# Optimization experiments

Measured on AMD Instinct MI355X. Metric: run time of the kernel, lower is better.

Reference implementation:

```python
import jax, jax.numpy as jnp
import numpy as np

EPS = 1e-8


def setup_inputs() -> dict:
    key = jax.random.key(0)
    k1, k2, k3, k4 = jax.random.split(key, 4)
    B, S, H, D, E = 2, 2048, 1024, 4096, 8
    x = jax.random.normal(k1, (B, S, H), dtype=jnp.float32)
    routing_weights = jax.random.uniform(k2, (B, S, E), dtype=jnp.float32)
    # xavier-uniform-like scale for the expert weight tensors
    lim_d = float(np.sqrt(6.0 / (H + D)))
    lim_u = float(np.sqrt(6.0 / (D + H)))
    down_weights = jax.random.uniform(k3, (E, H, D), dtype=jnp.float32, minval=-lim_d, maxval=lim_d)
    up_weights = jax.random.uniform(k4, (E, D, H), dtype=jnp.float32, minval=-lim_u, maxval=lim_u)
    down_biases = jnp.zeros((E, D), dtype=jnp.float32)
    return {
        "x": x,
        "routing_weights": routing_weights,
        "down_weights": down_weights,
        "down_biases": down_biases,
        "up_weights": up_weights,
        "top_k": 2,
    }


def reference(x, routing_weights, down_weights, down_biases, up_weights, top_k):
    """SmearExpert.forward with routing_strategy='top_k_sparse' (3D routing weights).
    Returns (output, sparse_weights) exactly as the torch module does."""
    B, S, H = x.shape
    E = down_weights.shape[0]

    # top-k sparsification + renormalization of the routing weights
    topk_w, topk_i = jax.lax.top_k(routing_weights, top_k)          # [B,S,k]
    sparse_w = (jax.nn.one_hot(topk_i, E, dtype=x.dtype) * topk_w[..., None]).sum(-2)  # [B,S,E]
    sparse_w = sparse_w / (sparse_w.sum(-1, keepdims=True) + EPS)

    x_flat = x.reshape(-1, H)              # [T,H]
    w_flat = sparse_w.reshape(-1, E)       # [T,E]

    # per-expert down-proj -> GELU(exact) -> up-proj, combined with routing weights
    # (tokens with zero weight contribute nothing, matching the masked torch path)
    out = jnp.zeros_like(x_flat)
    for e in range(E):
        z = jax.nn.gelu(x_flat @ down_weights[e] + down_biases[e], approximate=False)  # [T,D]
        out = out + (z @ up_weights[e]) * w_flat[:, e:e + 1]
    return out.reshape(B, S, H), sparse_w
```

## Files before the change

kernel.cpp:

```cpp
#include <hip/hip_runtime.h>
#include <stdint.h>

#define T_TOK 4096
#define HDIM  1024
#define DDIM  4096
#define NEXP  8

typedef unsigned short ushort_t;
typedef __attribute__((ext_vector_type(8))) short bf16x8;
typedef __attribute__((ext_vector_type(4))) float f32x4;

__device__ __forceinline__ float bf2f(ushort_t b) {
  return __uint_as_float(((unsigned int)b) << 16);
}
__device__ __forceinline__ unsigned int f2bf(float f) {
  unsigned int u = __float_as_uint(f);
  return (u + 0x7fffu + ((u >> 16) & 1u)) >> 16;
}

__device__ __forceinline__ void gld16(const void* g, void* l) {
  __builtin_amdgcn_global_load_lds(
      (const __attribute__((address_space(1))) unsigned int*)g,
      (__attribute__((address_space(3))) unsigned int*)l, 16, 0, 0);
}

__global__ void k_init(int* counts) {
  if (threadIdx.x < NEXP) counts[threadIdx.x] = 0;
}

__global__ void k_route(const float* __restrict__ rw, float* __restrict__ sw_out,
                        int* counts, int* inv_e, int* inv_p, float* inv_w,
                        int* tokA) {
  int t = blockIdx.x * 256 + threadIdx.x;
  if (t >= T_TOK) return;
  float v[NEXP];
#pragma unroll
  for (int e = 0; e < NEXP; e++) v[e] = rw[t * NEXP + e];
  int i0 = 0; float m0 = v[0];
#pragma unroll
  for (int e = 1; e < NEXP; e++) if (v[e] > m0) { m0 = v[e]; i0 = e; }
  int i1 = -1; float m1 = -1e30f;
#pragma unroll
  for (int e = 0; e < NEXP; e++) if (e != i0 && v[e] > m1) { m1 = v[e]; i1 = e; }
  float s = m0 + m1 + 1e-8f;
  float w0 = m0 / s, w1 = m1 / s;
#pragma unroll
  for (int e = 0; e < NEXP; e++) {
    float w = (e == i0) ? w0 : ((e == i1) ? w1 : 0.0f);
    sw_out[t * NEXP + e] = w;
  }
  int p0 = atomicAdd(&counts[i0], 1);
  int p1 = atomicAdd(&counts[i1], 1);
  tokA[i0 * T_TOK + p0] = t;
  tokA[i1 * T_TOK + p1] = t;
  inv_e[t * 2] = i0; inv_e[t * 2 + 1] = i1;
  inv_p[t * 2] = p0; inv_p[t * 2 + 1] = p1;
  inv_w[t * 2] = w0; inv_w[t * 2 + 1] = w1;
}

__global__ void k_offsets(const int* counts, int* offsets) {
  int acc = 0;
  for (int e = 0; e < NEXP; e++) { offsets[e] = acc; acc += counts[e]; }
}

__global__ __launch_bounds__(256)
void k_cvtx(const float* __restrict__ x, ushort_t* __restrict__ xb) {
  size_t i = (size_t)blockIdx.x * 256 + threadIdx.x;
  float4 f0 = ((const float4*)x)[i * 2];
  float4 f1 = ((const float4*)x)[i * 2 + 1];
  uint4 o;
  o.x = f2bf(f0.x) | (f2bf(f0.y) << 16);
  o.y = f2bf(f0.z) | (f2bf(f0.w) << 16);
  o.z = f2bf(f1.x) | (f2bf(f1.y) << 16);
  o.w = f2bf(f1.z) | (f2bf(f1.w) << 16);
  ((uint4*)xb)[i] = o;
}

template <int KDIM, int NDIM>
__global__ __launch_bounds__(256)
void k_cvtw(const float* __restrict__ W, ushort_t* __restrict__ Wt) {
  constexpr int KT = KDIM / 64;
  __shared__ __align__(16) ushort_t lds[64 * 256];
  const int ekt = blockIdx.y;
  const int e  = ekt / KT;
  const int kt = ekt % KT;
  const int n0 = blockIdx.x * 256;
  const int t  = threadIdx.x;
  const int wv = t >> 6;
  const int ln = t & 63;
  const float* src = W + (size_t)e * KDIM * NDIM + (size_t)(kt * 64) * NDIM + n0;
#pragma unroll
  for (int it = 0; it < 16; ++it) {
    int r = it * 4 + wv;
    float4 f = *(const float4*)(src + (size_t)r * NDIM + ln * 4);
    uint2 o;
    o.x = f2bf(f.x) | (f2bf(f.y) << 16);
    o.y = f2bf(f.z) | (f2bf(f.w) << 16);
    *(uint2*)(lds + r * 256 + ln * 4) = o;
  }
  __syncthreads();
  ushort_t* dst = Wt + ((size_t)ekt * NDIM + n0 + t) * 64;
  const int sw = t & 7;
#pragma unroll
  for (int g = 0; g < 8; ++g) {
    unsigned int h0 = lds[(g * 8 + 0) * 256 + t];
    unsigned int h1 = lds[(g * 8 + 1) * 256 + t];
    unsigned int h2 = lds[(g * 8 + 2) * 256 + t];
    unsigned int h3 = lds[(g * 8 + 3) * 256 + t];
    unsigned int h4 = lds[(g * 8 + 4) * 256 + t];
    unsigned int h5 = lds[(g * 8 + 5) * 256 + t];
    unsigned int h6 = lds[(g * 8 + 6) * 256 + t];
    unsigned int h7 = lds[(g * 8 + 7) * 256 + t];
    uint4 o;
    o.x = h0 | (h1 << 16);
    o.y = h2 | (h3 << 16);
    o.z = h4 | (h5 << 16);
    o.w = h6 | (h7 << 16);
    *(uint4*)(dst + (g ^ sw) * 8) = o;
  }
}

template <int KDIM, int NDIM, bool DOWN>
__global__ __launch_bounds__(256, 3)
void k_gemm(const ushort_t* __restrict__ Asrc, const ushort_t* __restrict__ Wt,
            const float* __restrict__ bias, const int* __restrict__ counts,
            const int* __restrict__ offsets, const int* __restrict__ tokA,
            ushort_t* __restrict__ Out) {
  constexpr int KT = KDIM / 64;
  __shared__ __align__(16) short a_sh[128 * 64];
  __shared__ __align__(16) short b_sh[128 * 64];
  const int e    = blockIdx.y >> 5;
  const int tile = blockIdx.y & 31;
  const int cnt  = counts[e];
  if (tile * 128 >= cnt) return;
  const int off_e = offsets[e];
  const int zbase = off_e + tile * 128;
  const int n0    = blockIdx.x * 128;
  const int tid   = threadIdx.x;
  const int wave  = tid >> 6;
  const int lane  = tid & 63;
  const int rgrp  = lane >> 3;
  const int lc    = lane & 7;

  const ushort_t* abase[4];
#pragma unroll
  for (int i = 0; i < 4; i++) {
    int rl = wave * 32 + i * 8 + rgrp;
    int ridx = tile * 128 + rl;
    int ridx_c = (ridx < cnt) ? ridx : tile * 128;
    size_t row;
    if constexpr (DOWN) row = (size_t)tokA[e * T_TOK + ridx_c];
    else                row = (size_t)(off_e + ridx_c);
    abase[i] = Asrc + row * KDIM + ((lc ^ (rl & 7)) * 8);
  }
  const ushort_t* bbase = Wt + ((size_t)e * KT * NDIM + n0) * 64 + wave * 2048 + lane * 8;
  char* a_seg = (char*)a_sh + wave * 4096;
  char* b_seg = (char*)b_sh + wave * 4096;

  const int lm   = lane & 15;
  const int quad = lane >> 4;

  f32x4 acc[8][2];
  const f32x4 zero = {0.0f, 0.0f, 0.0f, 0.0f};
#pragma unroll
  for (int mf = 0; mf < 8; mf++)
#pragma unroll
    for (int nf = 0; nf < 2; nf++) acc[mf][nf] = zero;

  for (int kt = 0; kt < KT; ++kt) {
#pragma unroll
    for (int it = 0; it < 4; ++it)
      gld16(abase[it] + kt * 64, a_seg + it * 1024);
    const ushort_t* bg = bbase + (size_t)kt * (NDIM * 64);
#pragma unroll
    for (int it = 0; it < 4; ++it)
      gld16(bg + it * 512, b_seg + it * 1024);
    __syncthreads();
#pragma unroll
    for (int ks = 0; ks < 2; ++ks) {
      bf16x8 af[8];
#pragma unroll
      for (int mf = 0; mf < 8; mf++) {
        int m = mf * 16 + lm;
        int cc = (ks * 4 + quad) ^ (lm & 7);
        af[mf] = *(const bf16x8*)(a_sh + m * 64 + cc * 8);
      }
      bf16x8 bfv[2];
#pragma unroll
      for (int nf = 0; nf < 2; nf++) {
        int n = wave * 32 + nf * 16 + lm;
        int cc = (ks * 4 + quad) ^ (lm & 7);
        bfv[nf] = *(const bf16x8*)(b_sh + n * 64 + cc * 8);
      }
#pragma unroll
      for (int mf = 0; mf < 8; mf++)
#pragma unroll
        for (int nf = 0; nf < 2; nf++)
          acc[mf][nf] = __builtin_amdgcn_mfma_f32_16x16x32_bf16(af[mf], bfv[nf], acc[mf][nf], 0, 0, 0);
    }
    __syncthreads();
  }

  float bv[2] = {0.0f, 0.0f};
  if constexpr (DOWN) {
#pragma unroll
    for (int nf = 0; nf < 2; nf++)
      bv[nf] = bias[e * NDIM + n0 + wave * 32 + nf * 16 + lm];
  }
  short* ep = ((wave & 2) ? b_sh : a_sh) + (wave & 1) * 4096;
#pragma unroll
  for (int mf = 0; mf < 8; mf++)
#pragma unroll
    for (int nf = 0; nf < 2; nf++)
#pragma unroll
      for (int r = 0; r < 4; r++) {
        float v = acc[mf][nf][r];
        if constexpr (DOWN) {
          float zv = v + bv[nf];
          v = 0.5f * zv * (1.0f + erff(zv * 0.70710678118654752f));
        }
        ep[(mf * 16 + quad * 4 + r) * 32 + nf * 16 + lm] = (short)f2bf(v);
      }
  __syncthreads();
#pragma unroll
  for (int it = 0; it < 8; ++it) {
    int row = it * 16 + (lane >> 2);
    uint4 v = *(const uint4*)(ep + row * 32 + (lane & 3) * 8);
    if (tile * 128 + row < cnt)
      *(uint4*)(Out + (size_t)(zbase + row) * NDIM + n0 + wave * 32 + (lane & 3) * 8) = v;
  }
}

__global__ void k_combine(const ushort_t* __restrict__ U, const int* __restrict__ inv_e,
                          const int* __restrict__ inv_p, const float* __restrict__ inv_w,
                          const int* __restrict__ offsets, float* __restrict__ out) {
  int gid = blockIdx.x * 256 + threadIdx.x;
  int t  = gid >> 7;
  int hc = (gid & 127) * 8;
  int e0 = inv_e[t * 2], e1 = inv_e[t * 2 + 1];
  size_t s0 = (size_t)offsets[e0] + inv_p[t * 2];
  size_t s1 = (size_t)offsets[e1] + inv_p[t * 2 + 1];
  float w0 = inv_w[t * 2], w1 = inv_w[t * 2 + 1];
  const ushort_t* u0 = U + s0 * HDIM + hc;
  const ushort_t* u1 = U + s1 * HDIM + hc;
  uint4 q0 = *(const uint4*)u0;
  uint4 q1 = *(const uint4*)u1;
  const ushort_t* a = (const ushort_t*)&q0;
  const ushort_t* b = (const ushort_t*)&q1;
  float4 o0, o1;
  o0.x = w0 * bf2f(a[0]) + w1 * bf2f(b[0]);
  o0.y = w0 * bf2f(a[1]) + w1 * bf2f(b[1]);
  o0.z = w0 * bf2f(a[2]) + w1 * bf2f(b[2]);
  o0.w = w0 * bf2f(a[3]) + w1 * bf2f(b[3]);
  o1.x = w0 * bf2f(a[4]) + w1 * bf2f(b[4]);
  o1.y = w0 * bf2f(a[5]) + w1 * bf2f(b[5]);
  o1.z = w0 * bf2f(a[6]) + w1 * bf2f(b[6]);
  o1.w = w0 * bf2f(a[7]) + w1 * bf2f(b[7]);
  float* op = out + (size_t)t * HDIM + hc;
  *(float4*)(op)     = o0;
  *(float4*)(op + 4) = o1;
}

extern "C" void kernel_launch(void* const* d_in, const int* in_sizes, int n_in,
                              void* d_out, int out_size, void* d_ws, size_t ws_size,
                              hipStream_t stream) {
  const float* x  = (const float*)d_in[0];
  const float* rw = (const float*)d_in[1];
  const float* wd = (const float*)d_in[2];
  const float* bd = (const float*)d_in[3];
  const float* wu = (const float*)d_in[4];
  float* out    = (float*)d_out;
  float* sw_out = out + (size_t)T_TOK * HDIM;

  char* ws = (char*)d_ws;
  int*      counts = (int*)(ws);
  int*      offs   = (int*)(ws + 64);
  int*      inv_e  = (int*)(ws + 128);
  int*      inv_p  = (int*)(ws + 128 + 32768);
  float*    inv_w  = (float*)(ws + 128 + 65536);
  int*      tokA   = (int*)(ws + 128 + 98304);
  size_t    base   = 262144;
  ushort_t* Z      = (ushort_t*)(ws + base);
  ushort_t* U      = (ushort_t*)(ws + base + 67108864);
  ushort_t* xbf    = (ushort_t*)(ws + base + 67108864 + 16777216);
  ushort_t* Wt     = (ushort_t*)(ws + base + 67108864 + 16777216 + 8388608);

  k_init<<<1, 64, 0, stream>>>(counts);
  k_route<<<T_TOK / 256, 256, 0, stream>>>(rw, sw_out, counts, inv_e, inv_p, inv_w, tokA);
  k_offsets<<<1, 1, 0, stream>>>(counts, offs);
  k_cvtx<<<T_TOK * HDIM / 8 / 256, 256, 0, stream>>>(x, xbf);
  k_cvtw<HDIM, DDIM><<<dim3(DDIM / 256, NEXP * (HDIM / 64)), 256, 0, stream>>>(wd, Wt);
  k_gemm<HDIM, DDIM, true><<<dim3(DDIM / 128, NEXP * 32), 256, 0, stream>>>(
      xbf, Wt, bd, counts, offs, tokA, Z);
  k_cvtw<DDIM, HDIM><<<dim3(HDIM / 256, NEXP * (DDIM / 64)), 256, 0, stream>>>(wu, Wt);
  k_gemm<DDIM, HDIM, false><<<dim3(HDIM / 128, NEXP * 32), 256, 0, stream>>>(
      Z, Wt, nullptr, counts, offs, tokA, U);
  k_combine<<<(T_TOK * HDIM / 8) / 256, 256, 0, stream>>>(U, inv_e, inv_p, inv_w, offs, out);
}
```

Measured before the change: 603.3 us.

## Split-K up-projection with atomics, fast GELU, block-local routing counts, XCD swizzle

The up-projection GEMM is split four ways along K and accumulates fp32 partials into a pre-zeroed buffer with atomicAdd. This raises the number of workgroups for the under-filled N=1024 GEMM, at the cost of atomic traffic and an extra zero-fill pass. Both GEMMs gain a workgroup index remap meant to spread tiles across XCDs. Exact erff is replaced by an Abramowitz-Stegun erf approximation using a hardware reciprocal and fast exp. Routing now counts per block in LDS, so each block does one global atomic per expert instead of one per token per expert.

Result: faster. 578.1 us (-4.2%).

```diff
diff --git a/kernel.cpp b/kernel.cpp
--- a/kernel.cpp
+++ b/kernel.cpp
@@ -18,6 +18,20 @@
   return (u + 0x7fffu + ((u >> 16) & 1u)) >> 16;
 }
 
+__device__ __forceinline__ float gelu_f(float z) {
+  float x  = fabsf(z) * 0.70710678118654752f;
+  float t  = __builtin_amdgcn_rcpf(__builtin_fmaf(0.3275911f, x, 1.0f));
+  float p  = t * (0.254829592f +
+             t * (-0.284496736f +
+             t * (1.421413741f +
+             t * (-1.453152027f +
+             t * 1.061405429f))));
+  float ex = __expf(-x * x);
+  float er = __builtin_fmaf(-p, ex, 1.0f);
+  er = copysignf(er, z);
+  return 0.5f * z * (1.0f + er);
+}
+
 __device__ __forceinline__ void gld16(const void* g, void* l) {
   __builtin_amdgcn_global_load_lds(
       (const __attribute__((address_space(1))) unsigned int*)g,
@@ -28,11 +42,15 @@
   if (threadIdx.x < NEXP) counts[threadIdx.x] = 0;
 }
 
-__global__ void k_route(const float* __restrict__ rw, float* __restrict__ sw_out,
-                        int* counts, int* inv_e, int* inv_p, float* inv_w,
-                        int* tokA) {
+__global__ __launch_bounds__(256)
+void k_route(const float* __restrict__ rw, float* __restrict__ sw_out,
+             int* counts, int* inv_e, int* inv_p, float* inv_w,
+             int* tokA) {
+  __shared__ int lcnt[NEXP];
+  __shared__ int lbase[NEXP];
   int t = blockIdx.x * 256 + threadIdx.x;
-  if (t >= T_TOK) return;
+  if (threadIdx.x < NEXP) lcnt[threadIdx.x] = 0;
+  __syncthreads();
   float v[NEXP];
 #pragma unroll
   for (int e = 0; e < NEXP; e++) v[e] = rw[t * NEXP + e];
@@ -49,8 +67,14 @@
     float w = (e == i0) ? w0 : ((e == i1) ? w1 : 0.0f);
     sw_out[t * NEXP + e] = w;
   }
-  int p0 = atomicAdd(&counts[i0], 1);
-  int p1 = atomicAdd(&counts[i1], 1);
+  int p0l = atomicAdd(&lcnt[i0], 1);
+  int p1l = atomicAdd(&lcnt[i1], 1);
+  __syncthreads();
+  if (threadIdx.x < NEXP)
+    lbase[threadIdx.x] = atomicAdd(&counts[threadIdx.x], lcnt[threadIdx.x]);
+  __syncthreads();
+  int p0 = lbase[i0] + p0l;
+  int p1 = lbase[i1] + p1l;
   tokA[i0 * T_TOK + p0] = t;
   tokA[i1 * T_TOK + p1] = t;
   inv_e[t * 2] = i0; inv_e[t * 2 + 1] = i1;
@@ -74,6 +98,11 @@
   o.z = f2bf(f1.x) | (f2bf(f1.y) << 16);
   o.w = f2bf(f1.z) | (f2bf(f1.w) << 16);
   ((uint4*)xb)[i] = o;
+}
+
+__global__ __launch_bounds__(256)
+void k_zero(float4* __restrict__ p) {
+  p[(size_t)blockIdx.x * 256 + threadIdx.x] = make_float4(0.f, 0.f, 0.f, 0.f);
 }
 
 template <int KDIM, int NDIM>
@@ -125,22 +154,36 @@
 void k_gemm(const ushort_t* __restrict__ Asrc, const ushort_t* __restrict__ Wt,
             const float* __restrict__ bias, const int* __restrict__ counts,
             const int* __restrict__ offsets, const int* __restrict__ tokA,
-            ushort_t* __restrict__ Out) {
-  constexpr int KT = KDIM / 64;
+            void* __restrict__ Out_) {
+  constexpr int KT_FULL = KDIM / 64;
+  constexpr int SPL     = DOWN ? 1 : 4;
+  constexpr int KTL     = KT_FULL / SPL;
+  constexpr int NX      = NDIM / 128;
+  constexpr int NY      = NEXP * 32 * SPL;
+  constexpr int NWG     = NX * NY;
   __shared__ __align__(16) short a_sh[128 * 64];
   __shared__ __align__(16) short b_sh[128 * 64];
-  const int e    = blockIdx.y >> 5;
-  const int tile = blockIdx.y & 31;
+
+  int flat    = blockIdx.y * NX + blockIdx.x;
+  int logical = (flat & 7) * (NWG / 8) + (flat >> 3);
+  const int bx = logical & (NX - 1);
+  const int by = logical / NX;
+
+  const int s    = DOWN ? 0 : (by & 3);
+  const int ey   = DOWN ? by : (by >> 2);
+  const int e    = ey >> 5;
+  const int tile = ey & 31;
   const int cnt  = counts[e];
   if (tile * 128 >= cnt) return;
   const int off_e = offsets[e];
   const int zbase = off_e + tile * 128;
-  const int n0    = blockIdx.x * 128;
+  const int n0    = bx * 128;
   const int tid   = threadIdx.x;
   const int wave  = tid >> 6;
   const int lane  = tid & 63;
   const int rgrp  = lane >> 3;
   const int lc    = lane & 7;
+  const int kofs  = s * (KDIM / SPL);
 
   const ushort_t* abase[4];
 #pragma unroll
@@ -151,9 +194,10 @@
     size_t row;
     if constexpr (DOWN) row = (size_t)tokA[e * T_TOK + ridx_c];
     else                row = (size_t)(off_e + ridx_c);
-    abase[i] = Asrc + row * KDIM + ((lc ^ (rl & 7)) * 8);
-  }
-  const ushort_t* bbase = Wt + ((size_t)e * KT * NDIM + n0) * 64 + wave * 2048 + lane * 8;
+    abase[i] = Asrc + row * KDIM + kofs + ((lc ^ (rl & 7)) * 8);
+  }
+  const ushort_t* bbase =
+      Wt + ((size_t)(e * KT_FULL + s * KTL) * NDIM + n0) * 64 + wave * 2048 + lane * 8;
   char* a_seg = (char*)a_sh + wave * 4096;
   char* b_seg = (char*)b_sh + wave * 4096;
 
@@ -167,7 +211,7 @@
 #pragma unroll
     for (int nf = 0; nf < 2; nf++) acc[mf][nf] = zero;
 
-  for (int kt = 0; kt < KT; ++kt) {
+  for (int kt = 0; kt < KTL; ++kt) {
 #pragma unroll
     for (int it = 0; it < 4; ++it)
       gld16(abase[it] + kt * 64, a_seg + it * 1024);
@@ -201,37 +245,48 @@
     __syncthreads();
   }
 
-  float bv[2] = {0.0f, 0.0f};
   if constexpr (DOWN) {
+    ushort_t* Out = (ushort_t*)Out_;
+    float bv[2];
 #pragma unroll
     for (int nf = 0; nf < 2; nf++)
       bv[nf] = bias[e * NDIM + n0 + wave * 32 + nf * 16 + lm];
-  }
-  short* ep = ((wave & 2) ? b_sh : a_sh) + (wave & 1) * 4096;
-#pragma unroll
-  for (int mf = 0; mf < 8; mf++)
-#pragma unroll
-    for (int nf = 0; nf < 2; nf++)
-#pragma unroll
-      for (int r = 0; r < 4; r++) {
-        float v = acc[mf][nf][r];
-        if constexpr (DOWN) {
-          float zv = v + bv[nf];
-          v = 0.5f * zv * (1.0f + erff(zv * 0.70710678118654752f));
+    short* ep = ((wave & 2) ? b_sh : a_sh) + (wave & 1) * 4096;
+#pragma unroll
+    for (int mf = 0; mf < 8; mf++)
+#pragma unroll
+      for (int nf = 0; nf < 2; nf++)
+#pragma unroll
+        for (int r = 0; r < 4; r++) {
+          float v = gelu_f(acc[mf][nf][r] + bv[nf]);
+          ep[(mf * 16 + quad * 4 + r) * 32 + nf * 16 + lm] = (short)f2bf(v);
         }
-        ep[(mf * 16 + quad * 4 + r) * 32 + nf * 16 + lm] = (short)f2bf(v);
+    __syncthreads();
+#pragma unroll
+    for (int it = 0; it < 8; ++it) {
+      int row = it * 16 + (lane >> 2);
+      uint4 v = *(const uint4*)(ep + row * 32 + (lane & 3) * 8);
+      if (tile * 128 + row < cnt)
+        *(uint4*)(Out + (size_t)(zbase + row) * NDIM + n0 + wave * 32 + (lane & 3) * 8) = v;
+    }
+  } else {
+    float* Out = (float*)Out_;
+#pragma unroll
+    for (int mf = 0; mf < 8; mf++)
+#pragma unroll
+      for (int nf = 0; nf < 2; nf++) {
+        int ncol = n0 + wave * 32 + nf * 16 + lm;
+#pragma unroll
+        for (int r = 0; r < 4; r++) {
+          int m = mf * 16 + quad * 4 + r;
+          if (tile * 128 + m < cnt)
+            atomicAdd(&Out[(size_t)(zbase + m) * NDIM + ncol], acc[mf][nf][r]);
+        }
       }
-  __syncthreads();
-#pragma unroll
-  for (int it = 0; it < 8; ++it) {
-    int row = it * 16 + (lane >> 2);
-    uint4 v = *(const uint4*)(ep + row * 32 + (lane & 3) * 8);
-    if (tile * 128 + row < cnt)
-      *(uint4*)(Out + (size_t)(zbase + row) * NDIM + n0 + wave * 32 + (lane & 3) * 8) = v;
-  }
-}
-
-__global__ void k_combine(const ushort_t* __restrict__ U, const int* __restrict__ inv_e,
+  }
+}
+
+__global__ void k_combine(const float* __restrict__ U, const int* __restrict__ inv_e,
                           const int* __restrict__ inv_p, const float* __restrict__ inv_w,
                           const int* __restrict__ offsets, float* __restrict__ out) {
   int gid = blockIdx.x * 256 + threadIdx.x;
@@ -241,21 +296,21 @@
   size_t s0 = (size_t)offsets[e0] + inv_p[t * 2];
   size_t s1 = (size_t)offsets[e1] + inv_p[t * 2 + 1];
   float w0 = inv_w[t * 2], w1 = inv_w[t * 2 + 1];
-  const ushort_t* u0 = U + s0 * HDIM + hc;
-  const ushort_t* u1 = U + s1 * HDIM + hc;
-  uint4 q0 = *(const uint4*)u0;
-  uint4 q1 = *(const uint4*)u1;
-  const ushort_t* a = (const ushort_t*)&q0;
-  const ushort_t* b = (const ushort_t*)&q1;
+  const float* u0 = U + s0 * HDIM + hc;
+  const float* u1 = U + s1 * HDIM + hc;
+  float4 a0 = ((const float4*)u0)[0];
+  float4 a1 = ((const float4*)u0)[1];
+  float4 b0 = ((const float4*)u1)[0];
+  float4 b1 = ((const float4*)u1)[1];
   float4 o0, o1;
-  o0.x = w0 * bf2f(a[0]) + w1 * bf2f(b[0]);
-  o0.y = w0 * bf2f(a[1]) + w1 * bf2f(b[1]);
-  o0.z = w0 * bf2f(a[2]) + w1 * bf2f(b[2]);
-  o0.w = w0 * bf2f(a[3]) + w1 * bf2f(b[3]);
-  o1.x = w0 * bf2f(a[4]) + w1 * bf2f(b[4]);
-  o1.y = w0 * bf2f(a[5]) + w1 * bf2f(b[5]);
-  o1.z = w0 * bf2f(a[6]) + w1 * bf2f(b[6]);
-  o1.w = w0 * bf2f(a[7]) + w1 * bf2f(b[7]);
+  o0.x = w0 * a0.x + w1 * b0.x;
+  o0.y = w0 * a0.y + w1 * b0.y;
+  o0.z = w0 * a0.z + w1 * b0.z;
+  o0.w = w0 * a0.w + w1 * b0.w;
+  o1.x = w0 * a1.x + w1 * b1.x;
+  o1.y = w0 * a1.y + w1 * b1.y;
+  o1.z = w0 * a1.z + w1 * b1.z;
+  o1.w = w0 * a1.w + w1 * b1.w;
   float* op = out + (size_t)t * HDIM + hc;
   *(float4*)(op)     = o0;
   *(float4*)(op + 4) = o1;
@@ -281,9 +336,9 @@
   int*      tokA   = (int*)(ws + 128 + 98304);
   size_t    base   = 262144;
   ushort_t* Z      = (ushort_t*)(ws + base);
-  ushort_t* U      = (ushort_t*)(ws + base + 67108864);
-  ushort_t* xbf    = (ushort_t*)(ws + base + 67108864 + 16777216);
-  ushort_t* Wt     = (ushort_t*)(ws + base + 67108864 + 16777216 + 8388608);
+  ushort_t* Wt     = (ushort_t*)(ws + base + 67108864);
+  ushort_t* xbf    = (ushort_t*)(ws + base + 134217728);
+  float*    U32    = (float*)(ws + base + 134217728);
 
   k_init<<<1, 64, 0, stream>>>(counts);
   k_route<<<T_TOK / 256, 256, 0, stream>>>(rw, sw_out, counts, inv_e, inv_p, inv_w, tokA);
@@ -291,9 +346,10 @@
   k_cvtx<<<T_TOK * HDIM / 8 / 256, 256, 0, stream>>>(x, xbf);
   k_cvtw<HDIM, DDIM><<<dim3(DDIM / 256, NEXP * (HDIM / 64)), 256, 0, stream>>>(wd, Wt);
   k_gemm<HDIM, DDIM, true><<<dim3(DDIM / 128, NEXP * 32), 256, 0, stream>>>(
-      xbf, Wt, bd, counts, offs, tokA, Z);
+      xbf, Wt, bd, counts, offs, tokA, (void*)Z);
   k_cvtw<DDIM, HDIM><<<dim3(HDIM / 256, NEXP * (DDIM / 64)), 256, 0, stream>>>(wu, Wt);
-  k_gemm<DDIM, HDIM, false><<<dim3(HDIM / 128, NEXP * 32), 256, 0, stream>>>(
-      Z, Wt, nullptr, counts, offs, tokA, U);
-  k_combine<<<(T_TOK * HDIM / 8) / 256, 256, 0, stream>>>(U, inv_e, inv_p, inv_w, offs, out);
-}
+  k_zero<<<(8192 * HDIM / 4) / 256, 256, 0, stream>>>((float4*)U32);
+  k_gemm<DDIM, HDIM, false><<<dim3(HDIM / 128, NEXP * 32 * 4), 256, 0, stream>>>(
+      Z, Wt, nullptr, counts, offs, tokA, (void*)U32);
+  k_combine<<<(T_TOK * HDIM / 8) / 256, 256, 0, stream>>>(U32, inv_e, inv_p, inv_w, offs, out);
+}
```
